# Kernel optimization log

Hardware: AMD Instinct MI355X
Metric: run time of the kernel (lower is better)

Reference implementation:

```python
import jax, jax.numpy as jnp
import numpy as np

B, S, D, H, DFF = 2, 2048, 768, 12, 3072
HD = D // H
LN_EPS = 1e-5


def _layernorm(x, g, b):
    mu = jnp.mean(x, axis=-1, keepdims=True)
    var = jnp.mean((x - mu) ** 2, axis=-1, keepdims=True)
    return (x - mu) * jax.lax.rsqrt(var + LN_EPS) * g + b


def setup_inputs() -> dict:
    key = jax.random.key(0)
    ks = jax.random.split(key, 16)
    s_d = 1.0 / np.sqrt(D)
    s_ff = 1.0 / np.sqrt(DFF)
    return {
        "x": jax.random.normal(ks[0], (B, S, D), jnp.float32),
        "alibi_bias": jax.random.normal(ks[1], (H, S, S), jnp.float32) * 0.1,
        "Wq": jax.random.normal(ks[2], (D, D), jnp.float32) * s_d,
        "bq": jnp.zeros((D,), jnp.float32),
        "Wk": jax.random.normal(ks[3], (D, D), jnp.float32) * s_d,
        "bk": jnp.zeros((D,), jnp.float32),
        "Wv": jax.random.normal(ks[4], (D, D), jnp.float32) * s_d,
        "bv": jnp.zeros((D,), jnp.float32),
        "Wo": jax.random.normal(ks[5], (D, D), jnp.float32) * s_d,
        "bo": jnp.zeros((D,), jnp.float32),
        "W1": jax.random.normal(ks[6], (D, DFF), jnp.float32) * s_d,
        "b1": jnp.zeros((DFF,), jnp.float32),
        "W2": jax.random.normal(ks[7], (DFF, D), jnp.float32) * s_ff,
        "b2": jnp.zeros((D,), jnp.float32),
        "g1": jnp.ones((D,), jnp.float32),
        "be1": jnp.zeros((D,), jnp.float32),
        "g2": jnp.ones((D,), jnp.float32),
        "be2": jnp.zeros((D,), jnp.float32),
    }


def reference(x, alibi_bias, Wq, bq, Wk, bk, Wv, bv, Wo, bo, W1, b1, W2, b2, g1, be1, g2, be2):
    # QKV projections -> (B, H, S, HD)
    def split_heads(t):
        return t.reshape(B, S, H, HD).transpose(0, 2, 1, 3)

    q = split_heads(x @ Wq + bq)
    k = split_heads(x @ Wk + bk)
    v = split_heads(x @ Wv + bv)

    # causal mask (S, S): -inf above diagonal
    causal = jnp.where(jnp.triu(jnp.ones((S, S), bool), k=1), -jnp.inf, 0.0).astype(x.dtype)
    mask = alibi_bias[None] + causal[None, None]  # (1, H, S, S) broadcast over batch

    scale = 1.0 / np.sqrt(HD)
    scores = jnp.einsum("bhqd,bhkd->bhqk", q, k) * scale + mask
    probs = jax.nn.softmax(scores, axis=-1)
    attn = jnp.einsum("bhqk,bhkd->bhqd", probs, v)  # (B, H, S, HD)
    attn = attn.transpose(0, 2, 1, 3).reshape(B, S, D)
    attn = attn @ Wo + bo

    x = _layernorm(x + attn, g1, be1)
    ff = jax.nn.relu(x @ W1 + b1) @ W2 + b2
    x = _layernorm(x + ff, g2, be2)
    return x
```

## Files before the change

kernel.cpp:

```cpp
#include <hip/hip_runtime.h>
#include <hip/hip_bf16.h>

#define BB 2
#define SS 2048
#define DD 768
#define HH 12
#define HD 64
#define DFF 3072
#define NROW (BB * SS)
#define QLD  2304
#define LN_EPS 1e-5f
#define NSPLIT 4

typedef __attribute__((ext_vector_type(8))) short bf16x8;
typedef __attribute__((ext_vector_type(4))) short bf16x4;
typedef __attribute__((ext_vector_type(4))) float f32x4;

__device__ __forceinline__ void gll16(const void* g, void* l) {
    __builtin_amdgcn_global_load_lds(
        (const __attribute__((address_space(1))) unsigned int*)g,
        (__attribute__((address_space(3))) unsigned int*)l,
        16, 0, 0);
}

__device__ __forceinline__ unsigned short bf16bits(float f) {
    __hip_bfloat16 h = __float2bfloat16(f);
    return *(unsigned short*)&h;
}

__device__ __forceinline__ float bf16tof(unsigned short u) {
    unsigned int ui = ((unsigned int)u) << 16;
    return __uint_as_float(ui);
}

__device__ __forceinline__ float block_sum(float v, float* red) {
    __syncthreads();
    #pragma unroll
    for (int off = 32; off > 0; off >>= 1) v += __shfl_down(v, off, 64);
    if ((threadIdx.x & 63) == 0) red[threadIdx.x >> 6] = v;
    __syncthreads();
    if (threadIdx.x == 0) red[0] = red[0] + red[1] + red[2] + red[3];
    __syncthreads();
    return red[0];
}

template<int TM, int TN>
__global__ __launch_bounds__(256) void mfma_gemm(
        const __hip_bfloat16* __restrict__ A, const __hip_bfloat16* __restrict__ BT,
        const float* __restrict__ bias, float* __restrict__ Cf,
        __hip_bfloat16* __restrict__ Cb,
        int N, int K, int relu, int bf16out, int qscale_cols) {
    constexpr int BK = 64;
    constexpr int MW = TM / 32;
    constexpr int NW = TN / 32;
    __shared__ __hip_bfloat16 a_s[TM * BK];
    __shared__ __hip_bfloat16 b_s[TN * BK];

    const int tid  = threadIdx.x;
    const int lane = tid & 63;
    const int wid  = tid >> 6;
    const int wm   = (wid & 1) * (TM / 2);
    const int wn   = (wid >> 1) * (TN / 2);
    const int qq   = lane & 15;
    const int quad = lane >> 4;
    const int m0 = blockIdx.y * TM;
    const int n0 = blockIdx.x * TN;

    const int r8   = lane >> 3;
    const int u8   = lane & 7;
    const int gcol = ((u8 ^ r8) << 3);

    f32x4 acc[MW][NW] = {};

    for (int k0 = 0; k0 < K; k0 += BK) {
        const __hip_bfloat16* Ag = A + (size_t)m0 * K + k0 + gcol;
        #pragma unroll
        for (int i = 0; i < TM / 32; i++) {
            const int row = i * 32 + wid * 8 + r8;
            gll16(Ag + (size_t)row * K, a_s + row * BK + u8 * 8);
        }
        const __hip_bfloat16* Bg = BT + (size_t)n0 * K + k0 + gcol;
        #pragma unroll
        for (int i = 0; i < TN / 32; i++) {
            const int row = i * 32 + wid * 8 + r8;
            gll16(Bg + (size_t)row * K, b_s + row * BK + u8 * 8);
        }
        __syncthreads();

        #pragma unroll
        for (int kh = 0; kh < 2; kh++) {
            const int ku = kh * 4 + quad;
            bf16x8 af[MW], bfr[NW];
            #pragma unroll
            for (int mi = 0; mi < MW; mi++) {
                const int row = wm + mi * 16 + qq;
                af[mi] = *(const bf16x8*)(a_s + row * BK + ((ku ^ (qq & 7)) << 3));
            }
            #pragma unroll
            for (int ni = 0; ni < NW; ni++) {
                const int row = wn + ni * 16 + qq;
                bfr[ni] = *(const bf16x8*)(b_s + row * BK + ((ku ^ (qq & 7)) << 3));
            }
            #pragma unroll
            for (int mi = 0; mi < MW; mi++)
                #pragma unroll
                for (int ni = 0; ni < NW; ni++)
                    acc[mi][ni] = __builtin_amdgcn_mfma_f32_16x16x32_bf16(
                            af[mi], bfr[ni], acc[mi][ni], 0, 0, 0);
        }
        __syncthreads();
    }

    #pragma unroll
    for (int mi = 0; mi < MW; mi++) {
        #pragma unroll
        for (int ni = 0; ni < NW; ni++) {
            const int col = n0 + wn + ni * 16 + qq;
            const float bv = bias[col];
            const float sc = (col < qscale_cols) ? 0.125f : 1.0f;
            #pragma unroll
            for (int r = 0; r < 4; r++) {
                const int row = m0 + wm + mi * 16 + quad * 4 + r;
                float v = acc[mi][ni][r] + bv;
                if (relu) v = fmaxf(v, 0.f);
                v *= sc;
                if (bf16out) Cb[(size_t)row * N + col] = __float2bfloat16(v);
                else         Cf[(size_t)row * N + col] = v;
            }
        }
    }
}

__device__ __forceinline__ void transpose_tile(
        const float* __restrict__ in, __hip_bfloat16* __restrict__ out,
        int K, int N, int tix, int tiy, float (*t)[33]) {
    const int n0 = tix * 32;
    const int k0 = tiy * 32;
    const int r = threadIdx.x >> 3;
    const int c = threadIdx.x & 7;
    float4 v = *(const float4*)&in[(size_t)(k0 + r) * N + n0 + c * 4];
    t[r][c * 4 + 0] = v.x;
    t[r][c * 4 + 1] = v.y;
    t[r][c * 4 + 2] = v.z;
    t[r][c * 4 + 3] = v.w;
    __syncthreads();
    union { unsigned short u[4]; uint2 w; } pk;
    #pragma unroll
    for (int j = 0; j < 4; j++) pk.u[j] = bf16bits(t[c * 4 + j][r]);
    *(uint2*)&out[(size_t)(n0 + r) * K + k0 + c * 4] = pk.w;
}

__global__ __launch_bounds__(256) void prep_kernel(
        const float* __restrict__ Wq, const float* __restrict__ Wk,
        const float* __restrict__ Wv, const float* __restrict__ Wo,
        const float* __restrict__ W1, const float* __restrict__ W2,
        const float* __restrict__ bq, const float* __restrict__ bk,
        const float* __restrict__ bv, const float* __restrict__ x,
        __hip_bfloat16* __restrict__ WqkvT, __hip_bfloat16* __restrict__ WoT,
        __hip_bfloat16* __restrict__ W1T, __hip_bfloat16* __restrict__ W2T,
        float* __restrict__ biasc, __hip_bfloat16* __restrict__ xb) {
    __shared__ float t[32][33];
    const int bx = blockIdx.x;
    if (bx < 2304) {
        const int wsel = bx / 576;
        const int r = bx - wsel * 576;
        const float* in = (wsel == 0) ? Wq : (wsel == 1) ? Wk : (wsel == 2) ? Wv : Wo;
        __hip_bfloat16* out = (wsel == 3) ? WoT : WqkvT + (size_t)wsel * DD * DD;
        transpose_tile(in, out, DD, DD, r % 24, r / 24, t);
    } else if (bx < 4608) {
        const int r = bx - 2304;
        transpose_tile(W1, W1T, DD, DFF, r % 96, r / 96, t);
    } else if (bx < 6912) {
        const int r = bx - 4608;
        transpose_tile(W2, W2T, DFF, DD, r % 24, r / 24, t);
    } else if (bx < 9984) {
        const int i = (bx - 6912) * 256 + threadIdx.x;
        float4 v = ((const float4*)x)[i];
        union { unsigned short u[4]; uint2 w; } pk;
        pk.u[0] = bf16bits(v.x); pk.u[1] = bf16bits(v.y);
        pk.u[2] = bf16bits(v.z); pk.u[3] = bf16bits(v.w);
        ((uint2*)xb)[i] = pk.w;
    } else {
        const int i = (bx - 9984) * 256 + threadIdx.x;
        if (i < QLD)
            biasc[i] = (i < DD) ? bq[i] : ((i < 2 * DD) ? bk[i - DD] : bv[i - 2 * DD]);
    }
}

__global__ __launch_bounds__(256) void flash_attn_kernel(
        const __hip_bfloat16* __restrict__ QKV, const float* __restrict__ alibi,
        __hip_bfloat16* __restrict__ Opart, float* __restrict__ ml) {
    const int qt = (int)(gridDim.x / NSPLIT) - 1 - (int)(blockIdx.x / NSPLIT);
    const int s  = blockIdx.x & (NSPLIT - 1);
    const int h  = blockIdx.y;
    const int b  = blockIdx.z;
    const int tid  = threadIdx.x;
    const int lane = tid & 63;
    const int w    = tid >> 6;
    const int qq   = lane & 15;
    const int quad = lane >> 4;
    const int q0   = qt * 64;

    __shared__ unsigned short K_s[64 * 72];
    __shared__ unsigned short V_t[64 * 72];
    __shared__ unsigned short P_t[4][16 * 72];

    const size_t qrow = ((size_t)(b * SS + q0 + w * 16 + qq)) * QLD + (size_t)h * HD;
    const bf16x8 qf0 = *(const bf16x8*)(QKV + qrow + quad * 8);
    const bf16x8 qf1 = *(const bf16x8*)(QKV + qrow + 32 + quad * 8);

    f32x4 O[4] = {};
    float m_i = -1e30f, l_i = 0.f;

    const float* alrow = alibi + ((size_t)h * SS + q0 + w * 16 + qq) * SS;
    const size_t kvrow0 = (size_t)(b * SS) * QLD + (size_t)h * HD + w * 16;
    const int lim = q0 + w * 16 + qq;

    for (int t = s; t * 64 <= q0; t += NSPLIT) {
        const int k0 = t * 64;
        __syncthreads();

        {
            const size_t kv = kvrow0 + (size_t)(k0 + lane) * QLD;
            bf16x8 kv0 = *(const bf16x8*)(QKV + DD + kv);
            bf16x8 kv1 = *(const bf16x8*)(QKV + DD + kv + 8);
            *(bf16x8*)&K_s[lane * 72 + w * 16]     = kv0;
            *(bf16x8*)&K_s[lane * 72 + w * 16 + 8] = kv1;
            bf16x8 vv0 = *(const bf16x8*)(QKV + 2 * DD + kv);
            bf16x8 vv1 = *(const bf16x8*)(QKV + 2 * DD + kv + 8);
            #pragma unroll
            for (int j = 0; j < 8; j++) {
                V_t[(w * 16 + j) * 72 + lane]     = vv0[j];
                V_t[(w * 16 + 8 + j) * 72 + lane] = vv1[j];
            }
        }
        __syncthreads();

        float4 av[4];
        #pragma unroll
        for (int c = 0; c < 4; c++)
            av[c] = *(const float4*)(alrow + k0 + c * 16 + quad * 4);

        __builtin_amdgcn_s_setprio(1);
        f32x4 S[4];
        #pragma unroll
        for (int c = 0; c < 4; c++) {
            f32x4 sacc = {};
            bf16x8 kf0 = *(const bf16x8*)&K_s[(c * 16 + qq) * 72 + quad * 8];
            bf16x8 kf1 = *(const bf16x8*)&K_s[(c * 16 + qq) * 72 + 32 + quad * 8];
            sacc = __builtin_amdgcn_mfma_f32_16x16x32_bf16(kf0, qf0, sacc, 0, 0, 0);
            sacc = __builtin_amdgcn_mfma_f32_16x16x32_bf16(kf1, qf1, sacc, 0, 0, 0);
            S[c] = sacc;
        }
        __builtin_amdgcn_s_setprio(0);

        float sv[16];
        float smax = -1e30f;
        const int klim = lim - k0;
        #pragma unroll
        for (int c = 0; c < 4; c++) {
            #pragma unroll
            for (int r = 0; r < 4; r++) {
                const int key = c * 16 + quad * 4 + r;
                float sc = S[c][r] + ((const float*)&av[c])[r];
                if (key > klim) sc = -1e30f;
                sv[c * 4 + r] = sc;
                smax = fmaxf(smax, sc);
            }
        }
        smax = fmaxf(smax, __shfl_xor(smax, 16));
        smax = fmaxf(smax, __shfl_xor(smax, 32));

        const float nm = fmaxf(m_i, smax);
        const float alpha = __expf(m_i - nm);
        float lsum = 0.f;
        #pragma unroll
        for (int i = 0; i < 16; i++) {
            const float e = __expf(sv[i] - nm);
            sv[i] = e;
            lsum += e;
        }
        lsum += __shfl_xor(lsum, 16);
        lsum += __shfl_xor(lsum, 32);
        l_i = l_i * alpha + lsum;
        m_i = nm;

        #pragma unroll
        for (int c = 0; c < 4; c++) {
            bf16x4 pk;
            #pragma unroll
            for (int r = 0; r < 4; r++) pk[r] = (short)bf16bits(sv[c * 4 + r]);
            *(bf16x4*)&P_t[w][qq * 72 + c * 16 + quad * 4] = pk;
        }

        #pragma unroll
        for (int r = 0; r < 4; r++) {
            const float ar = __shfl(alpha, quad * 4 + r);
            #pragma unroll
            for (int d = 0; d < 4; d++) O[d][r] *= ar;
        }

        const bf16x8 pf0 = *(const bf16x8*)&P_t[w][qq * 72 + quad * 8];
        const bf16x8 pf1 = *(const bf16x8*)&P_t[w][qq * 72 + 32 + quad * 8];
        __builtin_amdgcn_s_setprio(1);
        #pragma unroll
        for (int d0 = 0; d0 < 4; d0++) {
            bf16x8 vf0 = *(const bf16x8*)&V_t[(d0 * 16 + qq) * 72 + quad * 8];
            bf16x8 vf1 = *(const bf16x8*)&V_t[(d0 * 16 + qq) * 72 + 32 + quad * 8];
            O[d0] = __builtin_amdgcn_mfma_f32_16x16x32_bf16(pf0, vf0, O[d0], 0, 0, 0);
            O[d0] = __builtin_amdgcn_mfma_f32_16x16x32_bf16(pf1, vf1, O[d0], 0, 0, 0);
        }
        __builtin_amdgcn_s_setprio(0);
    }

    if (quad == 0) {
        float* mlp = ml + (((size_t)(b * SS + q0 + w * 16 + qq) * HH + h) * NSPLIT + s) * 2;
        mlp[0] = m_i;
        mlp[1] = l_i;
    }
    #pragma unroll
    for (int r = 0; r < 4; r++) {
        const int row = q0 + w * 16 + quad * 4 + r;
        __hip_bfloat16* op = Opart +
            (((size_t)(b * SS + row) * HH + h) * NSPLIT + s) * 64 + qq;
        op[0]  = __float2bfloat16(O[0][r]);
        op[16] = __float2bfloat16(O[1][r]);
        op[32] = __float2bfloat16(O[2][r]);
        op[48] = __float2bfloat16(O[3][r]);
    }
}

__global__ __launch_bounds__(256) void attn_combine_kernel(
        const __hip_bfloat16* __restrict__ Opart, const float* __restrict__ ml,
        __hip_bfloat16* __restrict__ attnb) {
    const int idx = blockIdx.x * 256 + threadIdx.x;
    const int rr  = idx / 96;
    const int rem = idx - rr * 96;
    const int h   = rem >> 3;
    const int d8  = (rem & 7) * 8;
    const size_t base = ((size_t)rr * HH + h) * NSPLIT;
    float ms[NSPLIT], ls[NSPLIT];
    float m = -1e30f;
    #pragma unroll
    for (int s = 0; s < NSPLIT; s++) {
        ms[s] = ml[(base + s) * 2];
        ls[s] = ml[(base + s) * 2 + 1];
        m = fmaxf(m, ms[s]);
    }
    float es[NSPLIT], denom = 0.f;
    #pragma unroll
    for (int s = 0; s < NSPLIT; s++) {
        es[s] = __expf(ms[s] - m);
        denom += ls[s] * es[s];
    }
    const float inv = 1.f / denom;
    float acc[8] = {};
    #pragma unroll
    for (int s = 0; s < NSPLIT; s++) {
        const bf16x8 o = *(const bf16x8*)(Opart + (base + s) * 64 + d8);
        #pragma unroll
        for (int j = 0; j < 8; j++)
            acc[j] += bf16tof((unsigned short)o[j]) * es[s];
    }
    union { unsigned short u[8]; bf16x8 v; } pk;
    #pragma unroll
    for (int j = 0; j < 8; j++) pk.u[j] = bf16bits(acc[j] * inv);
    *(bf16x8*)(attnb + (size_t)rr * DD + h * 64 + d8) = pk.v;
}

__global__ __launch_bounds__(256) void ln_kernel(
        const float* __restrict__ a, const float* __restrict__ r,
        const float* __restrict__ g, const float* __restrict__ beta,
        float* __restrict__ outf, __hip_bfloat16* __restrict__ outb) {
    const int row = blockIdx.x;
    const int tid = threadIdx.x;
    __shared__ float red[64];

    float vals[3];
    float s = 0.f;
    #pragma unroll
    for (int i = 0; i < 3; i++) {
        const int col = i * 256 + tid;
        float t = a[(size_t)row * DD + col] + r[(size_t)row * DD + col];
        vals[i] = t;
        s += t;
    }
    const float mean = block_sum(s, red) * (1.f / DD);

    float s2 = 0.f;
    #pragma unroll
    for (int i = 0; i < 3; i++) {
        float d = vals[i] - mean;
        s2 += d * d;
    }
    const float var = block_sum(s2, red) * (1.f / DD);
    const float rstd = rsqrtf(var + LN_EPS);

    #pragma unroll
    for (int i = 0; i < 3; i++) {
        const int col = i * 256 + tid;
        const float o = (vals[i] - mean) * rstd * g[col] + beta[col];
        outf[(size_t)row * DD + col] = o;
        if (outb) outb[(size_t)row * DD + col] = __float2bfloat16(o);
    }
}

extern "C" void kernel_launch(void* const* d_in, const int* in_sizes, int n_in,
                              void* d_out, int out_size, void* d_ws, size_t ws_size,
                              hipStream_t stream) {
    const float* x     = (const float*)d_in[0];
    const float* alibi = (const float*)d_in[1];
    const float* Wq = (const float*)d_in[2];
    const float* bq = (const float*)d_in[3];
    const float* Wk = (const float*)d_in[4];
    const float* bk = (const float*)d_in[5];
    const float* Wv = (const float*)d_in[6];
    const float* bv = (const float*)d_in[7];
    const float* Wo = (const float*)d_in[8];
    const float* bo = (const float*)d_in[9];
    const float* W1 = (const float*)d_in[10];
    const float* b1 = (const float*)d_in[11];
    const float* W2 = (const float*)d_in[12];
    const float* b2 = (const float*)d_in[13];
    const float* g1 = (const float*)d_in[14];
    const float* be1 = (const float*)d_in[15];
    const float* g2 = (const float*)d_in[16];
    const float* be2 = (const float*)d_in[17];
    float* out = (float*)d_out;

    char* p = (char*)d_ws;
    auto alloc = [&](size_t bytes) { char* r = p; p += (bytes + 255) & ~(size_t)255; return r; };
    __hip_bfloat16* WqkvT = (__hip_bfloat16*)alloc((size_t)QLD * DD * 2);
    __hip_bfloat16* WoT   = (__hip_bfloat16*)alloc((size_t)DD * DD * 2);
    __hip_bfloat16* W1T   = (__hip_bfloat16*)alloc((size_t)DFF * DD * 2);
    __hip_bfloat16* W2T   = (__hip_bfloat16*)alloc((size_t)DD * DFF * 2);
    float*          biasc = (float*)alloc((size_t)QLD * 4);
    __hip_bfloat16* xb    = (__hip_bfloat16*)alloc((size_t)NROW * DD * 2);
    __hip_bfloat16* qkvb  = (__hip_bfloat16*)alloc((size_t)NROW * DFF * 2);
    __hip_bfloat16* attnb = (__hip_bfloat16*)alloc((size_t)NROW * DD * 2);
    float*          proj  = (float*)alloc((size_t)NROW * DD * 4);
    float*          ln1   = (float*)alloc((size_t)NROW * DD * 4);
    __hip_bfloat16* ln1b  = xb;
    __hip_bfloat16* ff1b  = qkvb;
    float*          ff2   = proj;

    __hip_bfloat16* Opart = (__hip_bfloat16*)proj;
    float*          mlbuf = (float*)xb;

    const dim3 blk(256);

    prep_kernel<<<dim3(9993), blk, 0, stream>>>(
            Wq, Wk, Wv, Wo, W1, W2, bq, bk, bv, x,
            WqkvT, WoT, W1T, W2T, biasc, xb);

    mfma_gemm<128, 96><<<dim3(QLD / 96, NROW / 128), blk, 0, stream>>>(
            xb, WqkvT, biasc, nullptr, qkvb, QLD, DD, 0, 1, DD);

    flash_attn_kernel<<<dim3(NSPLIT * (SS / 64), HH, BB), blk, 0, stream>>>(
            qkvb, alibi, Opart, mlbuf);
    attn_combine_kernel<<<dim3(NROW * 96 / 256), blk, 0, stream>>>(
            Opart, mlbuf, attnb);

    mfma_gemm<64, 64><<<dim3(DD / 64, NROW / 64), blk, 0, stream>>>(
            attnb, WoT, bo, proj, nullptr, DD, DD, 0, 0, 0);

    ln_kernel<<<dim3(NROW), blk, 0, stream>>>(x, proj, g1, be1, ln1, ln1b);

    mfma_gemm<128, 128><<<dim3(DFF / 128, NROW / 128), blk, 0, stream>>>(
            ln1b, W1T, b1, nullptr, ff1b, DFF, DD, 1, 1, 0);
    mfma_gemm<64, 64><<<dim3(DD / 64, NROW / 64), blk, 0, stream>>>(
            ff1b, W2T, b2, ff2, nullptr, DD, DFF, 0, 0, 0);

    ln_kernel<<<dim3(NROW), blk, 0, stream>>>(ln1, ff2, g2, be2, out, nullptr);
}
```

Before: 484.4 us.

## Balance causal attention splits per query tile and split-K the FF2 GEMM

The flash attention grid now assigns a variable number of KV splits per query tile (4 for late tiles down to 1 for early tiles), so blocks do more even work and fewer blocks are launched. The combine kernel reads only the valid partials. The FF2 GEMM (K=3072) is split into two K halves across blockIdx.z, writing two fp32 partial buffers that the second layernorm sums together with the bias. This raises parallelism for the long-K GEMM at the cost of extra fp32 traffic and a larger workspace.

```diff
diff --git a/kernel.cpp b/kernel.cpp
--- a/kernel.cpp
+++ b/kernel.cpp
@@ -49,12 +49,20 @@
         const __hip_bfloat16* __restrict__ A, const __hip_bfloat16* __restrict__ BT,
         const float* __restrict__ bias, float* __restrict__ Cf,
         __hip_bfloat16* __restrict__ Cb,
-        int N, int K, int relu, int bf16out, int qscale_cols) {
+        int N, int Klen, int lda, int relu, int bf16out, int qscale_cols,
+        int ksplit) {
     constexpr int BK = 64;
     constexpr int MW = TM / 32;
     constexpr int NW = TN / 32;
     __shared__ __hip_bfloat16 a_s[TM * BK];
     __shared__ __hip_bfloat16 b_s[TN * BK];
+
+    if (ksplit > 0) {
+        const int koff = blockIdx.z * ksplit;
+        A  += koff;
+        BT += koff;
+        Cf += (size_t)blockIdx.z * NROW * N;
+    }
 
     const int tid  = threadIdx.x;
     const int lane = tid & 63;
@@ -72,18 +80,18 @@
 
     f32x4 acc[MW][NW] = {};
 
-    for (int k0 = 0; k0 < K; k0 += BK) {
-        const __hip_bfloat16* Ag = A + (size_t)m0 * K + k0 + gcol;
+    for (int k0 = 0; k0 < Klen; k0 += BK) {
+        const __hip_bfloat16* Ag = A + (size_t)m0 * lda + k0 + gcol;
         #pragma unroll
         for (int i = 0; i < TM / 32; i++) {
             const int row = i * 32 + wid * 8 + r8;
-            gll16(Ag + (size_t)row * K, a_s + row * BK + u8 * 8);
-        }
-        const __hip_bfloat16* Bg = BT + (size_t)n0 * K + k0 + gcol;
+            gll16(Ag + (size_t)row * lda, a_s + row * BK + u8 * 8);
+        }
+        const __hip_bfloat16* Bg = BT + (size_t)n0 * lda + k0 + gcol;
         #pragma unroll
         for (int i = 0; i < TN / 32; i++) {
             const int row = i * 32 + wid * 8 + r8;
-            gll16(Bg + (size_t)row * K, b_s + row * BK + u8 * 8);
+            gll16(Bg + (size_t)row * lda, b_s + row * BK + u8 * 8);
         }
         __syncthreads();
 
@@ -116,7 +124,7 @@
         #pragma unroll
         for (int ni = 0; ni < NW; ni++) {
             const int col = n0 + wn + ni * 16 + qq;
-            const float bv = bias[col];
+            const float bv = bias ? bias[col] : 0.f;
             const float sc = (col < qscale_cols) ? 0.125f : 1.0f;
             #pragma unroll
             for (int r = 0; r < 4; r++) {
@@ -190,8 +198,13 @@
 __global__ __launch_bounds__(256) void flash_attn_kernel(
         const __hip_bfloat16* __restrict__ QKV, const float* __restrict__ alibi,
         __hip_bfloat16* __restrict__ Opart, float* __restrict__ ml) {
-    const int qt = (int)(gridDim.x / NSPLIT) - 1 - (int)(blockIdx.x / NSPLIT);
-    const int s  = blockIdx.x & (NSPLIT - 1);
+    const int rb = blockIdx.x;
+    int qt, s, ns;
+    if (rb < 32)      { qt = 31 - (rb >> 2);              s = rb & 3;         ns = 4; }
+    else if (rb < 56) { const int r2 = rb - 32; qt = 23 - r2 / 3; s = r2 % 3; ns = 3; }
+    else if (rb < 72) { const int r2 = rb - 56; qt = 15 - (r2 >> 1); s = r2 & 1; ns = 2; }
+    else              { qt = 7 - (rb - 72);               s = 0;              ns = 1; }
+
     const int h  = blockIdx.y;
     const int b  = blockIdx.z;
     const int tid  = threadIdx.x;
@@ -216,7 +229,7 @@
     const size_t kvrow0 = (size_t)(b * SS) * QLD + (size_t)h * HD + w * 16;
     const int lim = q0 + w * 16 + qq;
 
-    for (int t = s; t * 64 <= q0; t += NSPLIT) {
+    for (int t = s; t <= qt; t += ns) {
         const int k0 = t * 64;
         __syncthreads();
 
@@ -338,29 +351,35 @@
     const int rem = idx - rr * 96;
     const int h   = rem >> 3;
     const int d8  = (rem & 7) * 8;
+    const int qt  = (rr & (SS - 1)) >> 6;
+    const int ns  = (qt >> 3) + 1;
     const size_t base = ((size_t)rr * HH + h) * NSPLIT;
     float ms[NSPLIT], ls[NSPLIT];
     float m = -1e30f;
     #pragma unroll
     for (int s = 0; s < NSPLIT; s++) {
-        ms[s] = ml[(base + s) * 2];
-        ls[s] = ml[(base + s) * 2 + 1];
-        m = fmaxf(m, ms[s]);
+        if (s < ns) {
+            ms[s] = ml[(base + s) * 2];
+            ls[s] = ml[(base + s) * 2 + 1];
+            m = fmaxf(m, ms[s]);
+        } else { ms[s] = -1e30f; ls[s] = 0.f; }
     }
     float es[NSPLIT], denom = 0.f;
     #pragma unroll
     for (int s = 0; s < NSPLIT; s++) {
-        es[s] = __expf(ms[s] - m);
+        es[s] = (s < ns) ? __expf(ms[s] - m) : 0.f;
         denom += ls[s] * es[s];
     }
     const float inv = 1.f / denom;
     float acc[8] = {};
     #pragma unroll
     for (int s = 0; s < NSPLIT; s++) {
-        const bf16x8 o = *(const bf16x8*)(Opart + (base + s) * 64 + d8);
-        #pragma unroll
-        for (int j = 0; j < 8; j++)
-            acc[j] += bf16tof((unsigned short)o[j]) * es[s];
+        if (s < ns) {
+            const bf16x8 o = *(const bf16x8*)(Opart + (base + s) * 64 + d8);
+            #pragma unroll
+            for (int j = 0; j < 8; j++)
+                acc[j] += bf16tof((unsigned short)o[j]) * es[s];
+        }
     }
     union { unsigned short u[8]; bf16x8 v; } pk;
     #pragma unroll
@@ -370,6 +389,7 @@
 
 __global__ __launch_bounds__(256) void ln_kernel(
         const float* __restrict__ a, const float* __restrict__ r,
+        const float* __restrict__ r2, const float* __restrict__ cb,
         const float* __restrict__ g, const float* __restrict__ beta,
         float* __restrict__ outf, __hip_bfloat16* __restrict__ outb) {
     const int row = blockIdx.x;
@@ -382,6 +402,8 @@
     for (int i = 0; i < 3; i++) {
         const int col = i * 256 + tid;
         float t = a[(size_t)row * DD + col] + r[(size_t)row * DD + col];
+        if (r2) t += r2[(size_t)row * DD + col];
+        if (cb) t += cb[col];
         vals[i] = t;
         s += t;
     }
@@ -440,9 +462,9 @@
     __hip_bfloat16* attnb = (__hip_bfloat16*)alloc((size_t)NROW * DD * 2);
     float*          proj  = (float*)alloc((size_t)NROW * DD * 4);
     float*          ln1   = (float*)alloc((size_t)NROW * DD * 4);
+    float*          ff2ab = (float*)alloc((size_t)2 * NROW * DD * 4);
     __hip_bfloat16* ln1b  = xb;
     __hip_bfloat16* ff1b  = qkvb;
-    float*          ff2   = proj;
 
     __hip_bfloat16* Opart = (__hip_bfloat16*)proj;
     float*          mlbuf = (float*)xb;
@@ -454,22 +476,26 @@
             WqkvT, WoT, W1T, W2T, biasc, xb);
 
     mfma_gemm<128, 96><<<dim3(QLD / 96, NROW / 128), blk, 0, stream>>>(
-            xb, WqkvT, biasc, nullptr, qkvb, QLD, DD, 0, 1, DD);
-
-    flash_attn_kernel<<<dim3(NSPLIT * (SS / 64), HH, BB), blk, 0, stream>>>(
+            xb, WqkvT, biasc, nullptr, qkvb, QLD, DD, DD, 0, 1, DD, 0);
+
+    flash_attn_kernel<<<dim3(80, HH, BB), blk, 0, stream>>>(
             qkvb, alibi, Opart, mlbuf);
     attn_combine_kernel<<<dim3(NROW * 96 / 256), blk, 0, stream>>>(
             Opart, mlbuf, attnb);
 
     mfma_gemm<64, 64><<<dim3(DD / 64, NROW / 64), blk, 0, stream>>>(
-            attnb, WoT, bo, proj, nullptr, DD, DD, 0, 0, 0);
-
-    ln_kernel<<<dim3(NROW), blk, 0, stream>>>(x, proj, g1, be1, ln1, ln1b);
+            attnb, WoT, bo, proj, nullptr, DD, DD, DD, 0, 0, 0, 0);
+
+    ln_kernel<<<dim3(NROW), blk, 0, stream>>>(
+            x, proj, nullptr, nullptr, g1, be1, ln1, ln1b);
 
     mfma_gemm<128, 128><<<dim3(DFF / 128, NROW / 128), blk, 0, stream>>>(
-            ln1b, W1T, b1, nullptr, ff1b, DFF, DD, 1, 1, 0);
-    mfma_gemm<64, 64><<<dim3(DD / 64, NROW / 64), blk, 0, stream>>>(
-            ff1b, W2T, b2, ff2, nullptr, DD, DFF, 0, 0, 0);
-
-    ln_kernel<<<dim3(NROW), blk, 0, stream>>>(ln1, ff2, g2, be2, out, nullptr);
-}
+            ln1b, W1T, b1, nullptr, ff1b, DFF, DD, DD, 1, 1, 0, 0);
+
+    mfma_gemm<64, 64><<<dim3(DD / 64, NROW / 64, 2), blk, 0, stream>>>(
+            ff1b, W2T, nullptr, ff2ab, nullptr, DD, DFF / 2, DFF, 0, 0, 0,
+            DFF / 2);
+
+    ln_kernel<<<dim3(NROW), blk, 0, stream>>>(
+            ln1, ff2ab, ff2ab + (size_t)NROW * DD, b2, g2, be2, out, nullptr);
+}
```

Measured after the change: 499.9 us. 1.03x slower.
